# Kernel tuning notes

Measured on AMD Instinct MI355X. Metric: run time of the kernel, lower is better.

The kernel has to match this reference:

```python
import jax, jax.numpy as jnp
import numpy as np

IN_DIM, OUT_DIM, H, K, N = 2048, 2048, 8192, 256, 4096


def _w_eff(codebook, idx, frozen_mask, int8_mask, int8_vals, w_float, alpha):
    looked = codebook[idx]
    merged = jnp.where(int8_mask, alpha * int8_vals, w_float)
    return jnp.where(frozen_mask, looked, merged)


def _c19(x, c_raw, rho_raw):
    c = jnp.maximum(c_raw, 0.1)
    rho = jnp.maximum(rho_raw, 0.0)
    L = 6.0 * c
    scaled = x / c
    n = jnp.floor(scaled)
    t = scaled - n
    h = t * (1.0 - t)
    # torch: n.long() % 2 == 0 -> +1 else -1 (python-style modulo, same as jnp.mod)
    sgn = jnp.where(jnp.mod(n.astype(jnp.int32), 2) == 0, 1.0, -1.0)
    interior = c * (sgn * h + rho * h * h)
    return jnp.where(x >= L, x - L, jnp.where(x <= -L, x + L, interior))


def setup_inputs() -> dict:
    key = jax.random.key(0)
    ks = jax.random.split(key, 16)
    x = jax.random.normal(ks[0], (N, IN_DIM), dtype=jnp.float32)
    codebook_W1 = jax.random.normal(ks[1], (K,), dtype=jnp.float32) * 0.02
    codebook_W2 = jax.random.normal(ks[2], (K,), dtype=jnp.float32) * 0.02
    W1_idx = jax.random.randint(ks[3], (IN_DIM, H), 0, K)
    W2_idx = jax.random.randint(ks[4], (H, OUT_DIM), 0, K)
    W1_frozen_mask = jax.random.bernoulli(ks[5], 0.5, (IN_DIM, H))
    W2_frozen_mask = jax.random.bernoulli(ks[6], 0.5, (H, OUT_DIM))
    W1_int8_mask = jax.random.bernoulli(ks[7], 0.25, (IN_DIM, H))
    W2_int8_mask = jax.random.bernoulli(ks[8], 0.25, (H, OUT_DIM))
    # quantized levels (stored as float32 buffers in the torch module)
    W1_int8 = jnp.round(jnp.clip(jax.random.normal(ks[9], (IN_DIM, H)) * 40.0, -127, 127))
    W2_int8 = jnp.round(jnp.clip(jax.random.normal(ks[10], (H, OUT_DIM)) * 40.0, -127, 127))
    W1_float = jax.random.normal(ks[11], (IN_DIM, H), dtype=jnp.float32) * 0.02
    W2_float = jax.random.normal(ks[12], (H, OUT_DIM), dtype=jnp.float32) * 0.02
    # alpha = max(|free float cells|)/127 as in __init__ (mask out frozen cells)
    a1 = jnp.maximum(jnp.abs(jnp.where(W1_frozen_mask, 0.0, W1_float)).max() / 127.0, 1e-6)
    a2 = jnp.maximum(jnp.abs(jnp.where(W2_frozen_mask, 0.0, W2_float)).max() / 127.0, 1e-6)
    b1 = jax.random.normal(ks[13], (H,), dtype=jnp.float32) * 0.01
    b2 = jax.random.normal(ks[14], (OUT_DIM,), dtype=jnp.float32) * 0.01
    db1 = jax.random.normal(ks[15], (H,), dtype=jnp.float32) * 0.01
    db2 = jax.random.normal(jax.random.fold_in(key, 99), (IN_DIM,), dtype=jnp.float32) * 0.01
    c_raw = jnp.full((H,), 1.0, dtype=jnp.float32)
    rho_raw = jnp.full((H,), 8.0, dtype=jnp.float32)
    return {
        "x": x, "codebook_W1": codebook_W1, "codebook_W2": codebook_W2,
        "W1_idx": W1_idx, "W2_idx": W2_idx,
        "W1_frozen_mask": W1_frozen_mask, "W2_frozen_mask": W2_frozen_mask,
        "W1_int8_mask": W1_int8_mask, "W2_int8_mask": W2_int8_mask,
        "W1_int8": W1_int8, "W2_int8": W2_int8,
        "W1_float": W1_float, "W2_float": W2_float,
        "alpha_free_W1": a1, "alpha_free_W2": a2,
        "b1": b1, "b2": b2, "db1": db1, "db2": db2,
        "c_raw": c_raw, "rho_raw": rho_raw,
    }


def reference(x, codebook_W1, codebook_W2, W1_idx, W2_idx,
              W1_frozen_mask, W2_frozen_mask, W1_int8_mask, W2_int8_mask,
              W1_int8, W2_int8, W1_float, W2_float,
              alpha_free_W1, alpha_free_W2, b1, b2, db1, db2, c_raw, rho_raw):
    W1 = _w_eff(codebook_W1, W1_idx, W1_frozen_mask, W1_int8_mask, W1_int8, W1_float, alpha_free_W1)
    W2 = _w_eff(codebook_W2, W2_idx, W2_frozen_mask, W2_int8_mask, W2_int8, W2_float, alpha_free_W2)
    # encode
    z = _c19(x @ W1 + b1, c_raw, rho_raw) @ W2 + b2          # [N, out_dim]
    # decode
    dec = (z @ W2.T + db1) @ W1.T + db2                      # [N, in_dim]
    return (dec, z)
```

## Files before the change

kernel.cpp:

```cpp
#include <hip/hip_runtime.h>

#define AS1 __attribute__((address_space(1)))
#define AS3 __attribute__((address_space(3)))

typedef __attribute__((ext_vector_type(8))) short short8;
typedef __attribute__((ext_vector_type(8))) float float8;
typedef __attribute__((ext_vector_type(8))) int int8v;
typedef __attribute__((ext_vector_type(4))) float f32x4;
typedef __attribute__((ext_vector_type(4))) unsigned short u16x4;

__device__ __forceinline__ unsigned short f2bf(float f) {
  union { float f; unsigned u; } v; v.f = f;
  return (unsigned short)((v.u + 0x7fffu + ((v.u >> 16) & 1u)) >> 16);
}

__device__ __forceinline__ void gload_lds16(const void* g, void* l) {
  __builtin_amdgcn_global_load_lds((const AS1 unsigned*)g, (AS3 unsigned*)l, 16, 0, 0);
}

#define MEMFENCE asm volatile("" ::: "memory")
#define BARRIER() do { MEMFENCE; __builtin_amdgcn_s_barrier(); MEMFENCE; } while (0)

__global__ void detect_fmt(const unsigned char* __restrict__ m, int* __restrict__ flag) {
  __shared__ int found;
  if (threadIdx.x == 0) found = 0;
  __syncthreads();
  for (int i = threadIdx.x; i < 4096; i += 256)
    if ((i & 3) != 0 && m[i] != 0) found = 1;
  __syncthreads();
  if (threadIdx.x == 0) flag[0] = found;
}

__global__ __launch_bounds__(256) void build_w2(
    const float* __restrict__ cb, const int* __restrict__ idx,
    const unsigned char* __restrict__ fz8, const unsigned char* __restrict__ im8,
    const float* __restrict__ i8v, const float* __restrict__ wf,
    const float* __restrict__ alpha_p, const int* __restrict__ flag_p,
    unsigned short* __restrict__ w_nat, unsigned short* __restrict__ w_t,
    int R, int C) {
  __shared__ float cbs[256];
  __shared__ float tile[64][65];
  const int t = threadIdx.x;
  cbs[t] = cb[t];
  const int rBase = blockIdx.y * 64, cBase = blockIdx.x * 64;
  const float alpha = alpha_p[0];
  const int isU8 = flag_p[0];
  __syncthreads();
#pragma unroll
  for (int p = 0; p < 2; ++p) {
    const int rl = p * 32 + (t >> 3);
    const int cl = (t & 7) * 8;
    const size_t off = (size_t)(rBase + rl) * C + cBase + cl;
    float8 wv = *(const float8*)(wf + off);
    float8 qv = *(const float8*)(i8v + off);
    int8v iv = *(const int8v*)(idx + off);
    unsigned fzm[8], imm[8];
    if (isU8) {
      unsigned long long fm = *(const unsigned long long*)(fz8 + off);
      unsigned long long im = *(const unsigned long long*)(im8 + off);
#pragma unroll
      for (int k = 0; k < 8; ++k) { fzm[k] = (fm >> (8 * k)) & 255ull; imm[k] = (im >> (8 * k)) & 255ull; }
    } else {
      int8v fv = *(const int8v*)((const int*)fz8 + off);
      int8v mv = *(const int8v*)((const int*)im8 + off);
#pragma unroll
      for (int k = 0; k < 8; ++k) { fzm[k] = fv[k]; imm[k] = mv[k]; }
    }
    short8 o;
#pragma unroll
    for (int k = 0; k < 8; ++k) {
      float r = fzm[k] ? cbs[iv[k] & 255] : (imm[k] ? alpha * qv[k] : wv[k]);
      o[k] = (short)f2bf(r);
      tile[rl][cl + k] = r;
    }
    *(short8*)(w_nat + off) = o;
  }
  __syncthreads();
#pragma unroll
  for (int p = 0; p < 2; ++p) {
    const int cl = p * 32 + (t >> 3);
    const int r0 = (t & 7) * 8;
    short8 o;
#pragma unroll
    for (int j = 0; j < 8; ++j) o[j] = (short)f2bf(tile[r0 + j][cl]);
    *(short8*)(w_t + (size_t)(cBase + cl) * R + rBase + r0) = o;
  }
}

__global__ __launch_bounds__(256) void cvt_bf16(const float* __restrict__ in,
                                                unsigned short* __restrict__ out, int n4) {
  int i = blockIdx.x * 256 + threadIdx.x;
  if (i < n4) {
    float4 v = ((const float4*)in)[i];
    u16x4 r;
    r.x = f2bf(v.x); r.y = f2bf(v.y); r.z = f2bf(v.z); r.w = f2bf(v.w);
    ((u16x4*)out)[i] = r;
  }
}

template <int MODE>
__global__ __launch_bounds__(512, 2) void gemm8(
    const unsigned short* __restrict__ A, const unsigned short* __restrict__ Bt,
    int M, int N, int K,
    const float* __restrict__ bias,
    const float* __restrict__ c_raw, const float* __restrict__ rho_raw,
    unsigned short* __restrict__ outB) {
  extern __shared__ unsigned short lds8[];
  const int t = threadIdx.x;
  const int l = t & 63, w = t >> 6;
  const int wm = w >> 2, wn = w & 3;
  const int lr = l & 15, q = l >> 4;

  const int nwg = gridDim.x;
  const int id = (blockIdx.x & 7) * (nwg >> 3) + (blockIdx.x >> 3);
  const int nbx = N >> 8;
  const int tileM = (id / nbx) * 256, tileN = (id % nbx) * 256;

  f32x4 acc[8][4];
#pragma unroll
  for (int mi = 0; mi < 8; ++mi)
#pragma unroll
    for (int ni = 0; ni < 4; ++ni) acc[mi][ni] = (f32x4){0.f, 0.f, 0.f, 0.f};

  const int srow = l >> 3, sslot = l & 7;
  const unsigned short* aSrc[2];
  const unsigned short* bSrc[2];
  int ldsOff[2];
#pragma unroll
  for (int i = 0; i < 2; ++i) {
    int rl = w * 16 + i * 8 + srow;
    int sl = sslot ^ (rl & 7);
    aSrc[i] = A + (size_t)(tileM + rl) * K + sl * 8;
    bSrc[i] = Bt + (size_t)(tileN + rl) * K + sl * 8;
    ldsOff[i] = (w * 2 + i) * 512;
  }
  const size_t dK = (size_t)128 * K;

#define STAGE_A0(buf, kt) { gload_lds16(aSrc[0] + (kt), lds8 + (buf)*32768 + 0*8192 + ldsOff[0]); \
                            gload_lds16(aSrc[1] + (kt), lds8 + (buf)*32768 + 0*8192 + ldsOff[1]); }
#define STAGE_A1(buf, kt) { gload_lds16(aSrc[0] + dK + (kt), lds8 + (buf)*32768 + 1*8192 + ldsOff[0]); \
                            gload_lds16(aSrc[1] + dK + (kt), lds8 + (buf)*32768 + 1*8192 + ldsOff[1]); }
#define STAGE_B0(buf, kt) { gload_lds16(bSrc[0] + (kt), lds8 + (buf)*32768 + 2*8192 + ldsOff[0]); \
                            gload_lds16(bSrc[1] + (kt), lds8 + (buf)*32768 + 2*8192 + ldsOff[1]); }
#define STAGE_B1(buf, kt) { gload_lds16(bSrc[0] + dK + (kt), lds8 + (buf)*32768 + 3*8192 + ldsOff[0]); \
                            gload_lds16(bSrc[1] + dK + (kt), lds8 + (buf)*32768 + 3*8192 + ldsOff[1]); }

  const int sw = (lr & 7) << 4;
  const int k0 = (q * 16) ^ sw;
  const int k1 = (64 + q * 16) ^ sw;
  const char* ldsc = (const char*)lds8;
  const int bRowBase = (wn & 1) * 64;

  const int nt = K >> 6;
  STAGE_A0(0, 0); STAGE_A1(0, 0); STAGE_B0(0, 0); STAGE_B1(0, 0);
  {
    int kt1 = (nt > 1) ? 64 : 0;
    STAGE_B0(1, kt1); STAGE_B1(1, kt1);
  }
  asm volatile("s_waitcnt vmcnt(4)" ::: "memory");
  BARRIER();

  short8 af[4][2], bf[4][2];
  for (int tt = 0; tt < nt; ++tt) {
    const int cur = tt & 1, nx = cur ^ 1;
    const int ktA = (tt + 1 < nt ? tt + 1 : 0) << 6;
    const int ktB = (tt + 2 < nt ? tt + 2 : 0) << 6;
    const int aB = cur * 65536 + wm * 16384;
    const int bB = cur * 65536 + 32768 + (wn >> 1) * 16384;

#pragma unroll
    for (int mi = 0; mi < 4; ++mi) {
      af[mi][0] = *(const short8*)(ldsc + aB + (mi * 16 + lr) * 128 + k0);
      af[mi][1] = *(const short8*)(ldsc + aB + (mi * 16 + lr) * 128 + k1);
    }
#pragma unroll
    for (int ni = 0; ni < 2; ++ni) {
      bf[ni][0] = *(const short8*)(ldsc + bB + (bRowBase + ni * 16 + lr) * 128 + k0);
      bf[ni][1] = *(const short8*)(ldsc + bB + (bRowBase + ni * 16 + lr) * 128 + k1);
    }
    STAGE_A0(nx, ktA);
    BARRIER();
    asm volatile("s_waitcnt lgkmcnt(0)" ::: "memory");
    __builtin_amdgcn_s_setprio(1);
#pragma unroll
    for (int mi = 0; mi < 4; ++mi)
#pragma unroll
      for (int ni = 0; ni < 2; ++ni) {
        acc[mi][ni] = __builtin_amdgcn_mfma_f32_16x16x32_bf16(af[mi][0], bf[ni][0], acc[mi][ni], 0, 0, 0);
        acc[mi][ni] = __builtin_amdgcn_mfma_f32_16x16x32_bf16(af[mi][1], bf[ni][1], acc[mi][ni], 0, 0, 0);
      }
    __builtin_amdgcn_s_setprio(0);
    BARRIER();

#pragma unroll
    for (int ni = 2; ni < 4; ++ni) {
      bf[ni][0] = *(const short8*)(ldsc + bB + (bRowBase + ni * 16 + lr) * 128 + k0);
      bf[ni][1] = *(const short8*)(ldsc + bB + (bRowBase + ni * 16 + lr) * 128 + k1);
    }
    STAGE_A1(nx, ktA);
    BARRIER();
    asm volatile("s_waitcnt lgkmcnt(0)" ::: "memory");
    __builtin_amdgcn_s_setprio(1);
#pragma unroll
    for (int mi = 0; mi < 4; ++mi)
#pragma unroll
      for (int ni = 2; ni < 4; ++ni) {
        acc[mi][ni] = __builtin_amdgcn_mfma_f32_16x16x32_bf16(af[mi][0], bf[ni][0], acc[mi][ni], 0, 0, 0);
        acc[mi][ni] = __builtin_amdgcn_mfma_f32_16x16x32_bf16(af[mi][1], bf[ni][1], acc[mi][ni], 0, 0, 0);
      }
    __builtin_amdgcn_s_setprio(0);
    BARRIER();

#pragma unroll
    for (int mi = 0; mi < 4; ++mi) {
      af[mi][0] = *(const short8*)(ldsc + aB + ((mi + 4) * 16 + lr) * 128 + k0);
      af[mi][1] = *(const short8*)(ldsc + aB + ((mi + 4) * 16 + lr) * 128 + k1);
    }
    STAGE_B0(cur, ktB);
    BARRIER();
    asm volatile("s_waitcnt lgkmcnt(0)" ::: "memory");
    __builtin_amdgcn_s_setprio(1);
#pragma unroll
    for (int mi = 0; mi < 4; ++mi)
#pragma unroll
      for (int ni = 2; ni < 4; ++ni) {
        acc[mi + 4][ni] = __builtin_amdgcn_mfma_f32_16x16x32_bf16(af[mi][0], bf[ni][0], acc[mi + 4][ni], 0, 0, 0);
        acc[mi + 4][ni] = __builtin_amdgcn_mfma_f32_16x16x32_bf16(af[mi][1], bf[ni][1], acc[mi + 4][ni], 0, 0, 0);
      }
    __builtin_amdgcn_s_setprio(0);
    BARRIER();

    STAGE_B1(cur, ktB);
    BARRIER();
    __builtin_amdgcn_s_setprio(1);
#pragma unroll
    for (int mi = 0; mi < 4; ++mi)
#pragma unroll
      for (int ni = 0; ni < 2; ++ni) {
        acc[mi + 4][ni] = __builtin_amdgcn_mfma_f32_16x16x32_bf16(af[mi][0], bf[ni][0], acc[mi + 4][ni], 0, 0, 0);
        acc[mi + 4][ni] = __builtin_amdgcn_mfma_f32_16x16x32_bf16(af[mi][1], bf[ni][1], acc[mi + 4][ni], 0, 0, 0);
      }
    __builtin_amdgcn_s_setprio(0);
    asm volatile("s_waitcnt vmcnt(4)" ::: "memory");
    BARRIER();
  }
#undef STAGE_A0
#undef STAGE_A1
#undef STAGE_B0
#undef STAGE_B1

#pragma unroll
  for (int ni = 0; ni < 4; ++ni) {
    const int col = tileN + wn * 64 + ni * 16 + lr;
    const float bv = bias[col];
    float cc = 0.f, rr = 0.f, L = 0.f;
    if constexpr (MODE == 0) {
      cc = fmaxf(c_raw[col], 0.1f);
      rr = fmaxf(rho_raw[col], 0.0f);
      L = 6.0f * cc;
    }
#pragma unroll
    for (int mi = 0; mi < 8; ++mi) {
      const int row0 = tileM + wm * 128 + mi * 16 + q * 4;
#pragma unroll
      for (int j = 0; j < 4; ++j) {
        float v = acc[mi][ni][j] + bv;
        size_t off = (size_t)(row0 + j) * N + col;
        if constexpr (MODE == 0) {
          float scaled = v / cc;
          float fn = floorf(scaled);
          float ttf = scaled - fn;
          float h = ttf * (1.0f - ttf);
          int ip = (int)fn;
          float sgn = (ip & 1) ? -1.0f : 1.0f;
          float interior = cc * (sgn * h + rr * h * h);
          float res = (v >= L) ? (v - L) : ((v <= -L) ? (v + L) : interior);
          outB[off] = f2bf(res);
        } else {
          outB[off] = f2bf(v);
        }
      }
    }
  }
}

template <int MODE>
__global__ __launch_bounds__(256) void gemm_bt(
    const unsigned short* __restrict__ A, const unsigned short* __restrict__ Bt,
    int M, int N, int K,
    const float* __restrict__ bias,
    float* __restrict__ outF, unsigned short* __restrict__ outB) {
  __shared__ __align__(16) unsigned short ldsA[128 * 64];
  __shared__ __align__(16) unsigned short ldsB[128 * 64];
  const int t = threadIdx.x;
  const int l = t & 63, w = t >> 6;
  const int wr = w >> 1, wc = w & 1;
  const int lr = l & 15, q = l >> 4;
  const int tileM = blockIdx.y * 128, tileN = blockIdx.x * 128;

  f32x4 acc[4][4];
#pragma unroll
  for (int mi = 0; mi < 4; ++mi)
#pragma unroll
    for (int ni = 0; ni < 4; ++ni) acc[mi][ni] = (f32x4){0.f, 0.f, 0.f, 0.f};

  const int chRow = l >> 3;
  const int subSlot = l & 7;
  const unsigned short* pa[4];
  const unsigned short* pb[4];
  unsigned short* la[4];
  unsigned short* lb[4];
#pragma unroll
  for (int i = 0; i < 4; ++i) {
    int chunk = 4 * w + i;
    int row = chunk * 8 + chRow;
    int sl = subSlot ^ (row & 7);
    pa[i] = A + (size_t)(tileM + row) * K + sl * 8;
    pb[i] = Bt + (size_t)(tileN + row) * K + sl * 8;
    la[i] = ldsA + chunk * 512;
    lb[i] = ldsB + chunk * 512;
  }
  int offA[2][4], offB[2][4];
#pragma unroll
  for (int kk = 0; kk < 2; ++kk)
#pragma unroll
    for (int i = 0; i < 4; ++i) {
      int rowA = wr * 64 + i * 16 + lr;
      offA[kk][i] = (rowA * 128 + kk * 64 + q * 16) ^ ((rowA & 7) << 4);
      int rowB = wc * 64 + i * 16 + lr;
      offB[kk][i] = (rowB * 128 + kk * 64 + q * 16) ^ ((rowB & 7) << 4);
    }

  for (int kt = 0; kt < K; kt += 64) {
#pragma unroll
    for (int i = 0; i < 4; ++i) gload_lds16(pa[i] + kt, la[i]);
#pragma unroll
    for (int i = 0; i < 4; ++i) gload_lds16(pb[i] + kt, lb[i]);
    __syncthreads();
#pragma unroll
    for (int kk = 0; kk < 2; ++kk) {
      short8 af[4], bfr[4];
#pragma unroll
      for (int mi = 0; mi < 4; ++mi)
        af[mi] = *(const short8*)((const char*)ldsA + offA[kk][mi]);
#pragma unroll
      for (int ni = 0; ni < 4; ++ni)
        bfr[ni] = *(const short8*)((const char*)ldsB + offB[kk][ni]);
#pragma unroll
      for (int mi = 0; mi < 4; ++mi)
#pragma unroll
        for (int ni = 0; ni < 4; ++ni)
          acc[mi][ni] = __builtin_amdgcn_mfma_f32_16x16x32_bf16(af[mi], bfr[ni], acc[mi][ni], 0, 0, 0);
    }
    __syncthreads();
  }

#pragma unroll
  for (int ni = 0; ni < 4; ++ni) {
    int col = tileN + wc * 64 + ni * 16 + lr;
    float bv = bias[col];
#pragma unroll
    for (int mi = 0; mi < 4; ++mi) {
      int row0 = tileM + wr * 64 + mi * 16 + q * 4;
#pragma unroll
      for (int j = 0; j < 4; ++j) {
        float v = acc[mi][ni][j] + bv;
        size_t off = (size_t)(row0 + j) * N + col;
        if constexpr (MODE == 1) {
          outF[off] = v;
          outB[off] = f2bf(v);
        } else {
          outF[off] = v;
        }
      }
    }
  }
}

extern "C" void kernel_launch(void* const* d_in, const int* in_sizes, int n_in,
                              void* d_out, int out_size, void* d_ws, size_t ws_size,
                              hipStream_t stream) {
  (void)in_sizes; (void)n_in; (void)out_size; (void)ws_size;
  const float* x = (const float*)d_in[0];
  const float* cb1 = (const float*)d_in[1];
  const float* cb2 = (const float*)d_in[2];
  const int* idx1 = (const int*)d_in[3];
  const int* idx2 = (const int*)d_in[4];
  const unsigned char* fz1 = (const unsigned char*)d_in[5];
  const unsigned char* fz2 = (const unsigned char*)d_in[6];
  const unsigned char* im1 = (const unsigned char*)d_in[7];
  const unsigned char* im2 = (const unsigned char*)d_in[8];
  const float* i8v1 = (const float*)d_in[9];
  const float* i8v2 = (const float*)d_in[10];
  const float* wf1 = (const float*)d_in[11];
  const float* wf2 = (const float*)d_in[12];
  const float* a1 = (const float*)d_in[13];
  const float* a2 = (const float*)d_in[14];
  const float* b1 = (const float*)d_in[15];
  const float* b2 = (const float*)d_in[16];
  const float* db1 = (const float*)d_in[17];
  const float* db2 = (const float*)d_in[18];
  const float* c_raw = (const float*)d_in[19];
  const float* rho_raw = (const float*)d_in[20];

  char* ws = (char*)d_ws;
  const size_t WSZ = 33554432;
  unsigned short* W1T = (unsigned short*)(ws + 0 * WSZ);
  unsigned short* W1N = (unsigned short*)(ws + 1 * WSZ);
  unsigned short* W2T = (unsigned short*)(ws + 2 * WSZ);
  unsigned short* W2N = (unsigned short*)(ws + 3 * WSZ);
  unsigned short* XB = (unsigned short*)(ws + 4 * WSZ);
  unsigned short* H = (unsigned short*)(ws + 4 * WSZ + 16777216);
  unsigned short* ZB = (unsigned short*)(ws + 4 * WSZ + 16777216 + 67108864);
  int* flag = (int*)(ws + 4 * WSZ + 16777216 + 67108864 + 16777216);
  float* dec = (float*)d_out;
  float* zf = (float*)d_out + 8388608;

  (void)hipFuncSetAttribute((const void*)gemm8<0>, hipFuncAttributeMaxDynamicSharedMemorySize, 131072);
  (void)hipFuncSetAttribute((const void*)gemm8<2>, hipFuncAttributeMaxDynamicSharedMemorySize, 131072);

  detect_fmt<<<1, 256, 0, stream>>>(fz1, flag);
  build_w2<<<dim3(8192 / 64, 2048 / 64), 256, 0, stream>>>(cb1, idx1, fz1, im1, i8v1, wf1, a1, flag, W1N, W1T, 2048, 8192);
  build_w2<<<dim3(2048 / 64, 8192 / 64), 256, 0, stream>>>(cb2, idx2, fz2, im2, i8v2, wf2, a2, flag, W2N, W2T, 8192, 2048);
  cvt_bf16<<<8192, 256, 0, stream>>>(x, XB, 2097152);

  gemm8<0><<<512, 512, 131072, stream>>>(XB, W1T, 4096, 8192, 2048, b1, c_raw, rho_raw, H);
  gemm_bt<1><<<dim3(16, 32), 256, 0, stream>>>(H, W2T, 4096, 2048, 8192, b2, zf, ZB);
  gemm8<2><<<512, 512, 131072, stream>>>(ZB, W2N, 4096, 8192, 2048, db1, nullptr, nullptr, H);
  gemm_bt<3><<<dim3(16, 32), 256, 0, stream>>>(H, W1N, 4096, 2048, 8192, db2, dec, nullptr);
}
```

Baseline: 1.302 ms.

## Run K=8192 GEMMs on pipelined 256x256 kernel with split-K and combine pass

Drops the simple single-buffered 128x128 gemm_bt kernel used for the two long-K GEMMs, z = H·W2 and dec = H'·W1ᵀ. They now run on the double-buffered 256x256 gemm8 kernel with a split-K of 2, which gives 256 workgroups from the 128 output tiles. Each K slice writes fp32 partials, one into the final output and one into a weight buffer that is no longer needed. A vectorised combine kernel then sums the partials, adds the bias and, for z, emits the bf16 copy. In exchange it adds extra fp32 partial traffic and two more launches, and it depends on the freed weight buffers not being read again.

```diff
diff --git a/kernel.cpp b/kernel.cpp
--- a/kernel.cpp
+++ b/kernel.cpp
@@ -98,13 +98,35 @@
   }
 }
 
-template <int MODE>
+template <int WITHB16>
+__global__ __launch_bounds__(256) void combine(
+    const float* __restrict__ p0, const float* __restrict__ p1,
+    const float* __restrict__ bias, float* __restrict__ outF,
+    unsigned short* __restrict__ outB, int Nmask, int n4) {
+  for (int i = blockIdx.x * 256 + threadIdx.x; i < n4; i += gridDim.x * 256) {
+    float4 a = ((const float4*)p0)[i];
+    float4 b = ((const float4*)p1)[i];
+    float4 bv = *(const float4*)(bias + ((i * 4) & Nmask));
+    float4 v;
+    v.x = a.x + b.x + bv.x; v.y = a.y + b.y + bv.y;
+    v.z = a.z + b.z + bv.z; v.w = a.w + b.w + bv.w;
+    ((float4*)outF)[i] = v;
+    if constexpr (WITHB16) {
+      u16x4 r;
+      r.x = f2bf(v.x); r.y = f2bf(v.y); r.z = f2bf(v.z); r.w = f2bf(v.w);
+      ((u16x4*)outB)[i] = r;
+    }
+  }
+}
+
+template <int MODE, int SPLIT>
 __global__ __launch_bounds__(512, 2) void gemm8(
     const unsigned short* __restrict__ A, const unsigned short* __restrict__ Bt,
     int M, int N, int K,
     const float* __restrict__ bias,
     const float* __restrict__ c_raw, const float* __restrict__ rho_raw,
-    unsigned short* __restrict__ outB) {
+    unsigned short* __restrict__ outB,
+    float* __restrict__ pF0, float* __restrict__ pF1) {
   extern __shared__ unsigned short lds8[];
   const int t = threadIdx.x;
   const int l = t & 63, w = t >> 6;
@@ -113,8 +135,12 @@
 
   const int nwg = gridDim.x;
   const int id = (blockIdx.x & 7) * (nwg >> 3) + (blockIdx.x >> 3);
+  int tileId, slice, kBase;
+  if constexpr (SPLIT == 2) { tileId = id >> 1; slice = id & 1; kBase = slice * (K >> 1); }
+  else { tileId = id; slice = 0; kBase = 0; }
   const int nbx = N >> 8;
-  const int tileM = (id / nbx) * 256, tileN = (id % nbx) * 256;
+  const int tileM = (tileId / nbx) * 256, tileN = (tileId % nbx) * 256;
+  const int Keff = K / SPLIT;
 
   f32x4 acc[8][4];
 #pragma unroll
@@ -130,8 +156,8 @@
   for (int i = 0; i < 2; ++i) {
     int rl = w * 16 + i * 8 + srow;
     int sl = sslot ^ (rl & 7);
-    aSrc[i] = A + (size_t)(tileM + rl) * K + sl * 8;
-    bSrc[i] = Bt + (size_t)(tileN + rl) * K + sl * 8;
+    aSrc[i] = A + (size_t)(tileM + rl) * K + kBase + sl * 8;
+    bSrc[i] = Bt + (size_t)(tileN + rl) * K + kBase + sl * 8;
     ldsOff[i] = (w * 2 + i) * 512;
   }
   const size_t dK = (size_t)128 * K;
@@ -151,7 +177,7 @@
   const char* ldsc = (const char*)lds8;
   const int bRowBase = (wn & 1) * 64;
 
-  const int nt = K >> 6;
+  const int nt = Keff >> 6;
   STAGE_A0(0, 0); STAGE_A1(0, 0); STAGE_B0(0, 0); STAGE_B1(0, 0);
   {
     int kt1 = (nt > 1) ? 64 : 0;
@@ -249,11 +275,13 @@
 #undef STAGE_B0
 #undef STAGE_B1
 
+  float* pOut = nullptr;
+  if constexpr (MODE == 4) pOut = slice ? pF1 : pF0;
 #pragma unroll
   for (int ni = 0; ni < 4; ++ni) {
     const int col = tileN + wn * 64 + ni * 16 + lr;
-    const float bv = bias[col];
-    float cc = 0.f, rr = 0.f, L = 0.f;
+    float bv = 0.f, cc = 0.f, rr = 0.f, L = 0.f;
+    if constexpr (MODE == 0 || MODE == 2) bv = bias[col];
     if constexpr (MODE == 0) {
       cc = fmaxf(c_raw[col], 0.1f);
       rr = fmaxf(rho_raw[col], 0.0f);
@@ -276,101 +304,10 @@
           float interior = cc * (sgn * h + rr * h * h);
           float res = (v >= L) ? (v - L) : ((v <= -L) ? (v + L) : interior);
           outB[off] = f2bf(res);
-        } else {
-          outB[off] = f2bf(v);
-        }
-      }
-    }
-  }
-}
-
-template <int MODE>
-__global__ __launch_bounds__(256) void gemm_bt(
-    const unsigned short* __restrict__ A, const unsigned short* __restrict__ Bt,
-    int M, int N, int K,
-    const float* __restrict__ bias,
-    float* __restrict__ outF, unsigned short* __restrict__ outB) {
-  __shared__ __align__(16) unsigned short ldsA[128 * 64];
-  __shared__ __align__(16) unsigned short ldsB[128 * 64];
-  const int t = threadIdx.x;
-  const int l = t & 63, w = t >> 6;
-  const int wr = w >> 1, wc = w & 1;
-  const int lr = l & 15, q = l >> 4;
-  const int tileM = blockIdx.y * 128, tileN = blockIdx.x * 128;
-
-  f32x4 acc[4][4];
-#pragma unroll
-  for (int mi = 0; mi < 4; ++mi)
-#pragma unroll
-    for (int ni = 0; ni < 4; ++ni) acc[mi][ni] = (f32x4){0.f, 0.f, 0.f, 0.f};
-
-  const int chRow = l >> 3;
-  const int subSlot = l & 7;
-  const unsigned short* pa[4];
-  const unsigned short* pb[4];
-  unsigned short* la[4];
-  unsigned short* lb[4];
-#pragma unroll
-  for (int i = 0; i < 4; ++i) {
-    int chunk = 4 * w + i;
-    int row = chunk * 8 + chRow;
-    int sl = subSlot ^ (row & 7);
-    pa[i] = A + (size_t)(tileM + row) * K + sl * 8;
-    pb[i] = Bt + (size_t)(tileN + row) * K + sl * 8;
-    la[i] = ldsA + chunk * 512;
-    lb[i] = ldsB + chunk * 512;
-  }
-  int offA[2][4], offB[2][4];
-#pragma unroll
-  for (int kk = 0; kk < 2; ++kk)
-#pragma unroll
-    for (int i = 0; i < 4; ++i) {
-      int rowA = wr * 64 + i * 16 + lr;
-      offA[kk][i] = (rowA * 128 + kk * 64 + q * 16) ^ ((rowA & 7) << 4);
-      int rowB = wc * 64 + i * 16 + lr;
-      offB[kk][i] = (rowB * 128 + kk * 64 + q * 16) ^ ((rowB & 7) << 4);
-    }
-
-  for (int kt = 0; kt < K; kt += 64) {
-#pragma unroll
-    for (int i = 0; i < 4; ++i) gload_lds16(pa[i] + kt, la[i]);
-#pragma unroll
-    for (int i = 0; i < 4; ++i) gload_lds16(pb[i] + kt, lb[i]);
-    __syncthreads();
-#pragma unroll
-    for (int kk = 0; kk < 2; ++kk) {
-      short8 af[4], bfr[4];
-#pragma unroll
-      for (int mi = 0; mi < 4; ++mi)
-        af[mi] = *(const short8*)((const char*)ldsA + offA[kk][mi]);
-#pragma unroll
-      for (int ni = 0; ni < 4; ++ni)
-        bfr[ni] = *(const short8*)((const char*)ldsB + offB[kk][ni]);
-#pragma unroll
-      for (int mi = 0; mi < 4; ++mi)
-#pragma unroll
-        for (int ni = 0; ni < 4; ++ni)
-          acc[mi][ni] = __builtin_amdgcn_mfma_f32_16x16x32_bf16(af[mi], bfr[ni], acc[mi][ni], 0, 0, 0);
-    }
-    __syncthreads();
-  }
-
-#pragma unroll
-  for (int ni = 0; ni < 4; ++ni) {
-    int col = tileN + wc * 64 + ni * 16 + lr;
-    float bv = bias[col];
-#pragma unroll
-    for (int mi = 0; mi < 4; ++mi) {
-      int row0 = tileM + wr * 64 + mi * 16 + q * 4;
-#pragma unroll
-      for (int j = 0; j < 4; ++j) {
-        float v = acc[mi][ni][j] + bv;
-        size_t off = (size_t)(row0 + j) * N + col;
-        if constexpr (MODE == 1) {
-          outF[off] = v;
+        } else if constexpr (MODE == 2) {
           outB[off] = f2bf(v);
         } else {
-          outF[off] = v;
+          pOut[off] = v;
         }
       }
     }
@@ -416,16 +353,19 @@
   float* dec = (float*)d_out;
   float* zf = (float*)d_out + 8388608;
 
-  (void)hipFuncSetAttribute((const void*)gemm8<0>, hipFuncAttributeMaxDynamicSharedMemorySize, 131072);
-  (void)hipFuncSetAttribute((const void*)gemm8<2>, hipFuncAttributeMaxDynamicSharedMemorySize, 131072);
+  (void)hipFuncSetAttribute((const void*)gemm8<0, 1>, hipFuncAttributeMaxDynamicSharedMemorySize, 131072);
+  (void)hipFuncSetAttribute((const void*)gemm8<2, 1>, hipFuncAttributeMaxDynamicSharedMemorySize, 131072);
+  (void)hipFuncSetAttribute((const void*)gemm8<4, 2>, hipFuncAttributeMaxDynamicSharedMemorySize, 131072);
 
   detect_fmt<<<1, 256, 0, stream>>>(fz1, flag);
   build_w2<<<dim3(8192 / 64, 2048 / 64), 256, 0, stream>>>(cb1, idx1, fz1, im1, i8v1, wf1, a1, flag, W1N, W1T, 2048, 8192);
   build_w2<<<dim3(2048 / 64, 8192 / 64), 256, 0, stream>>>(cb2, idx2, fz2, im2, i8v2, wf2, a2, flag, W2N, W2T, 8192, 2048);
   cvt_bf16<<<8192, 256, 0, stream>>>(x, XB, 2097152);
 
-  gemm8<0><<<512, 512, 131072, stream>>>(XB, W1T, 4096, 8192, 2048, b1, c_raw, rho_raw, H);
-  gemm_bt<1><<<dim3(16, 32), 256, 0, stream>>>(H, W2T, 4096, 2048, 8192, b2, zf, ZB);
-  gemm8<2><<<512, 512, 131072, stream>>>(ZB, W2N, 4096, 8192, 2048, db1, nullptr, nullptr, H);
-  gemm_bt<3><<<dim3(16, 32), 256, 0, stream>>>(H, W1N, 4096, 2048, 8192, db2, dec, nullptr);
-}
+  gemm8<0, 1><<<512, 512, 131072, stream>>>(XB, W1T, 4096, 8192, 2048, b1, c_raw, rho_raw, H, nullptr, nullptr);
+  gemm8<4, 2><<<256, 512, 131072, stream>>>(H, W2T, 4096, 2048, 8192, nullptr, nullptr, nullptr, nullptr, zf, (float*)W1T);
+  combine<1><<<2048, 256, 0, stream>>>(zf, (float*)W1T, b2, zf, ZB, 2047, 2097152);
+  gemm8<2, 1><<<512, 512, 131072, stream>>>(ZB, W2N, 4096, 8192, 2048, db1, nullptr, nullptr, H, nullptr, nullptr);
+  gemm8<4, 2><<<256, 512, 131072, stream>>>(H, W1N, 4096, 2048, 8192, nullptr, nullptr, nullptr, nullptr, dec, (float*)W2T);
+  combine<0><<<2048, 256, 0, stream>>>(dec, (float*)W2T, db2, dec, nullptr, 2047, 2097152);
+}
```

Result: faster. 1.183 ms (-9.1%).
